# Kernel optimization log

Hardware: AMD Instinct MI355X
Metric: run time of the kernel (lower is better)

The kernel has to match this reference:

```python
import jax, jax.numpy as jnp
import numpy as np

B, C, H, T, K = 32, 128, 512, 8192, 512


def setup_inputs() -> dict:
    key = jax.random.key(0)
    ks = jax.random.split(key, 4)
    s = 0.02
    return {
        "x": jax.random.normal(ks[0], (B, C, T), dtype=jnp.float32),
        "up_w": jax.random.normal(ks[1], (H, C), dtype=jnp.float32) * s,
        "up_b": jnp.zeros((H,), jnp.float32),
        "sal_w": jax.random.normal(ks[2], (H, C), dtype=jnp.float32) * s,
        "sal_b": jnp.zeros((H,), jnp.float32),
        "down_w": jax.random.normal(ks[3], (C, H), dtype=jnp.float32) * s,
        "down_b": jnp.zeros((C,), jnp.float32),
        "k_sparse": K,
    }


def reference(x, up_w, up_b, sal_w, sal_b, down_w, down_b, k_sparse):
    b = x.shape[0]
    # 1x1 Conv1d == per-timestep GEMM
    sig = jnp.einsum('bct,hc->bht', x, up_w) + up_b[None, :, None]   # [B,H,T]
    sal = jnp.einsum('bct,hc->bht', x, sal_w) + sal_b[None, :, None]  # [B,H,T]
    # global softmax over flattened (H*T) per batch item
    flat = jax.nn.softmax(sal.reshape(b, -1), axis=-1)                # [B,H*T]
    # k-sparse: keep top-k values, zero everything else
    vals, idx = jax.lax.top_k(flat, k_sparse)                          # [B,K]
    sparse = jnp.zeros_like(flat).at[jnp.arange(b)[:, None], idx].set(vals)
    sal_sparse = sparse.reshape(sig.shape)                             # [B,H,T]
    gated = sig * sal_sparse                                           # [B,H,T]
    out = jnp.einsum('bht,ch->bct', gated, down_w) + down_b[None, :, None]
    return out
```

## Files before the change

### kernel.cpp

```cpp
#include <hip/hip_runtime.h>
#include <hip/hip_bf16.h>
#include <math.h>

#define BB 32
#define CC 128
#define HH 512
#define TT 8192
#define KMAX 512

#define NBIN 2048
#define CANDCAP 4096
#define HOTCAP 32768
#define TILES 2048
#define TLCAP 256
#define HFLOOR 0.6f
#define BW (0.875f / 2048.0f)
#define INVBW (2048.0f / 0.875f)
#define DELTA_C2 6e-3f
#define DELTA_C1 1.2e-2f

#define N_HIST 0
#define N_SUMEXP 262144
#define N_CANDCNT 262400
#define N_TILECNT 262528
#define N_ZERO 270720
#define N_TAU 270848
#define N_SELCNT 270976
#define N_CELLMAX 271360
#define N_TLIST 8659968
#define N_CANDVAL 10757120
#define N_CANDIDX 11805696
#define N_SELIDX 12329984
#define N_SELVAL 12395520
#define N_SWB 12461056
#define N_XF 12592128
#define N_DWT 79700992
#define N_NEED 79963136

#define O_HIST 0
#define O_SUMEXP 262144
#define O_CANDCNT 262400
#define O_HOTCNT 262528
#define O_ZERO 262656
#define O_TAU 262656
#define O_SELCNT 262784
#define O_CELLMAX 263168
#define O_HOTLIST 8651776
#define O_CANDVAL 8782848
#define O_CANDIDX 9831424
#define O_SELIDX 10355712
#define O_SELVAL 10421248

typedef __attribute__((ext_vector_type(8))) short short8;
typedef __attribute__((ext_vector_type(16))) float f32x16;
typedef __attribute__((address_space(3))) unsigned int lds_u32;
typedef const __attribute__((address_space(1))) unsigned int glb_u32;


__global__ void prep_w(const float* __restrict__ sw, short* __restrict__ swb) {
  int i = blockIdx.x * 256 + threadIdx.x;
  int m = i & 31, u = (i >> 5) & 1, kc = (i >> 6) & 7, w = (i >> 9) & 3, by = i >> 11;
  int h = by * 128 + w * 32 + m;
  int c0 = kc * 16 + u * 8;
  float4 f0 = *(const float4*)(sw + (size_t)h * CC + c0);
  float4 f1 = *(const float4*)(sw + (size_t)h * CC + c0 + 4);
  union { __hip_bfloat162 h2; unsigned u; } p0, p1, p2, p3;
  p0.h2 = __float22bfloat162_rn(make_float2(f0.x, f0.y));
  p1.h2 = __float22bfloat162_rn(make_float2(f0.z, f0.w));
  p2.h2 = __float22bfloat162_rn(make_float2(f1.x, f1.y));
  p3.h2 = __float22bfloat162_rn(make_float2(f1.z, f1.w));
  *(uint4*)(swb + (size_t)i * 8) = make_uint4(p0.u, p1.u, p2.u, p3.u);
}

__global__ void prep_dwt(const float* __restrict__ dw, float* __restrict__ dwt) {
  int i = blockIdx.x * 256 + threadIdx.x;
  int c = i & 127, h = i >> 7;
  dwt[(size_t)h * CC + c] = dw[(size_t)c * HH + h];
}

__global__ __launch_bounds__(256) void prep_xt(const float* __restrict__ x,
                                               short* __restrict__ xf) {
  __shared__ float Lt[128 * 128];
  int tid = threadIdx.x;
  int b = blockIdx.y, bx = blockIdx.x, t0g = bx * 128;
  const float* xb = x + (size_t)b * CC * TT;
  {
    int cq = tid >> 5, tq = tid & 31, t0 = tq * 4;
#pragma unroll
    for (int p = 0; p < 4; p++) {
      int c0 = p * 32 + cq * 4;
      float r0[4], r1[4], r2[4], r3[4];
      *(float4*)r0 = *(const float4*)(xb + (size_t)(c0 + 0) * TT + t0g + t0);
      *(float4*)r1 = *(const float4*)(xb + (size_t)(c0 + 1) * TT + t0g + t0);
      *(float4*)r2 = *(const float4*)(xb + (size_t)(c0 + 2) * TT + t0g + t0);
      *(float4*)r3 = *(const float4*)(xb + (size_t)(c0 + 3) * TT + t0g + t0);
#pragma unroll
      for (int j = 0; j < 4; j++) {
        int t = t0 + j;
        int addr = t * 128 + ((((c0 >> 2) ^ (t & 31)) << 2));
        *(float4*)&Lt[addr] = make_float4(r0[j], r1[j], r2[j], r3[j]);
      }
    }
  }
  __syncthreads();
  int u = tid & 1, m = (tid >> 1) & 31, nt = (tid >> 6) & 3;
  int t = nt * 32 + m;
  short* dst = xf + ((size_t)b * 64 + bx) * 16384 + nt * 4096 + u * 256 + m * 8;
#pragma unroll
  for (int kc = 0; kc < 8; kc++) {
    int c0 = kc * 16 + u * 8;
    float4 f0 = *(float4*)&Lt[t * 128 + ((((c0 >> 2) ^ (t & 31)) << 2))];
    float4 f1 = *(float4*)&Lt[t * 128 + (((((c0 + 4) >> 2) ^ (t & 31)) << 2))];
    union { __hip_bfloat162 h2; unsigned u; } p0, p1, p2, p3;
    p0.h2 = __float22bfloat162_rn(make_float2(f0.x, f0.y));
    p1.h2 = __float22bfloat162_rn(make_float2(f0.z, f0.w));
    p2.h2 = __float22bfloat162_rn(make_float2(f1.x, f1.y));
    p3.h2 = __float22bfloat162_rn(make_float2(f1.z, f1.w));
    *(uint4*)(dst + kc * 512) = make_uint4(p0.u, p1.u, p2.u, p3.u);
  }
}

__global__ __launch_bounds__(256) void pass_a_lds(const short* __restrict__ xf,
                                                  const short* __restrict__ swb,
                                                  const float* __restrict__ sb,
                                                  float* __restrict__ cellmax,
                                                  int* __restrict__ hist,
                                                  double* __restrict__ sumexp) {
  __shared__ short Xs[16384];
  __shared__ double sered[4];
  int tid = threadIdx.x;
  int w = tid >> 6, lane = tid & 63, m = lane & 31, u = lane >> 5;
  int id = blockIdx.x, b = blockIdx.y;
  int bx = ((id >> 5) << 3) | (id & 7);
  int by = (id >> 3) & 3;

  const short* xsl = xf + ((size_t)b * 64 + bx) * 16384;
  {
    const short* gs = xsl + w * 4096 + lane * 8;
    short* ls = &Xs[w * 4096];
#pragma unroll
    for (int i = 0; i < 8; i++) {
      __builtin_amdgcn_global_load_lds((glb_u32*)(gs + i * 512),
                                       (lds_u32*)(ls + i * 512), 16, 0, 0);
    }
  }

  const short* wb_ = swb + (size_t)(by * 4 + w) * 4096 + u * 256 + m * 8;
  short8 afr[8];
#pragma unroll
  for (int kc = 0; kc < 8; kc++) afr[kc] = *(const short8*)(wb_ + kc * 512);

  __syncthreads();

  f32x16 acc0, acc1, acc2, acc3;
#pragma unroll
  for (int r = 0; r < 16; r++) { acc0[r] = 0.f; acc1[r] = 0.f; acc2[r] = 0.f; acc3[r] = 0.f; }

  const short* xr = &Xs[u * 256 + m * 8];
#pragma unroll
  for (int kc = 0; kc < 8; kc++) {
    short8 b0 = *(const short8*)(xr + kc * 512);
    short8 b1 = *(const short8*)(xr + 4096 + kc * 512);
    short8 b2 = *(const short8*)(xr + 8192 + kc * 512);
    short8 b3 = *(const short8*)(xr + 12288 + kc * 512);
    acc0 = __builtin_amdgcn_mfma_f32_32x32x16_bf16(afr[kc], b0, acc0, 0, 0, 0);
    acc1 = __builtin_amdgcn_mfma_f32_32x32x16_bf16(afr[kc], b1, acc1, 0, 0, 0);
    acc2 = __builtin_amdgcn_mfma_f32_32x32x16_bf16(afr[kc], b2, acc2, 0, 0, 0);
    acc3 = __builtin_amdgcn_mfma_f32_32x32x16_bf16(afr[kc], b3, acc3, 0, 0, 0);
  }

  int h0 = by * 128;
  float tmax = -1e30f;
  float se = 0.f;
#define EPI(ACC)                                                              \
  {                                                                           \
    _Pragma("unroll") for (int g = 0; g < 4; g++) {                           \
      float bias4[4];                                                         \
      *(float4*)bias4 = *(const float4*)&sb[h0 + w * 32 + g * 8 + u * 4];     \
      _Pragma("unroll") for (int q = 0; q < 4; q++) {                         \
        float s = ACC[g * 4 + q] + bias4[q];                                  \
        tmax = fmaxf(tmax, s);                                                \
        se += __expf(s);                                                      \
        if (s >= HFLOOR) {                                                    \
          int bin = (int)((s - HFLOOR) * INVBW);                              \
          if (bin > NBIN - 1) bin = NBIN - 1;                                 \
          atomicAdd(&hist[b * NBIN + bin], 1);                                \
        }                                                                     \
      }                                                                       \
    }                                                                         \
  }
  EPI(acc0) EPI(acc1) EPI(acc2) EPI(acc3)
#undef EPI
  int cid = ((b * 4 + by) * 64 + bx) * 256 + tid;
  cellmax[cid] = tmax;
  double sed = (double)se;
#pragma unroll
  for (int mm = 1; mm < 64; mm <<= 1) sed += __shfl_xor(sed, mm);
  if (lane == 0) sered[w] = sed;
  __syncthreads();
  if (tid == 0) atomicAdd(&sumexp[b], sered[0] + sered[1] + sered[2] + sered[3]);
}

__global__ void pass_b(const int* __restrict__ hist, float* __restrict__ tau,
                       const int* __restrict__ kptr) {
  __shared__ int hsh[NBIN];
  __shared__ int ps[256];
  int b = blockIdx.x, tid = threadIdx.x;
  int part = 0;
#pragma unroll
  for (int j = 0; j < 8; j++) {
    int v = hist[b * NBIN + tid * 8 + j];
    hsh[tid * 8 + j] = v;
    part += v;
  }
  ps[tid] = part;
  __syncthreads();
  if (tid == 0) {
    int k = kptr[0];
    if (k < 1) k = 1;
    if (k > KMAX) k = KMAX;
    long cum = 0;
    float tv = HFLOOR;
    for (int i = 255; i >= 0; i--) {
      if (cum + ps[i] >= k) {
        long r = k - cum;
        long c2 = 0;
        for (int j = 7; j >= 0; j--) {
          c2 += hsh[i * 8 + j];
          if (c2 >= r) { tv = HFLOOR + (i * 8 + j) * BW; break; }
        }
        break;
      }
      cum += ps[i];
    }
    tau[b] = tv;
  }
}

__global__ void pass_c1_fast(const float* __restrict__ cellmax, const float* __restrict__ tau,
                             int* __restrict__ tilecnt, int* __restrict__ tlist) {
  int i = blockIdx.x * blockDim.x + threadIdx.x;
  float v = cellmax[i];
  int b = i >> 16;
  if (v >= tau[b] - DELTA_C1) {
    int tile = (b << 6) | ((i >> 8) & 63);
    int pos = atomicAdd(&tilecnt[tile], 1);
    if (pos < TLCAP) tlist[tile * TLCAP + pos] = i;
  }
}

__global__ __launch_bounds__(512, 2) void pass_c2_fast(
    const float* __restrict__ x, const float* __restrict__ sw,
    const float* __restrict__ sb, const float* __restrict__ tau,
    const int* __restrict__ tilecnt, const int* __restrict__ tlist,
    int* __restrict__ candcnt, double* __restrict__ candval, int* __restrict__ candidx) {
  __shared__ float Xt[128 * 132];
  int tile = blockIdx.x;
  int b = tile >> 6, bx = tile & 63;
  int cnt = tilecnt[tile];
  if (cnt <= 0) return;
  if (cnt > TLCAP) cnt = TLCAP;
  int tid = threadIdx.x;
  {
    int cq = tid >> 5, tq = tid & 31, t4 = tq * 4;
    int sw4 = ((t4 >> 5) & 3) << 2;
    const float* xb = x + (size_t)b * CC * TT + bx * 128;
#pragma unroll
    for (int p = 0; p < 8; p++) {
      int c = p * 16 + cq;
      float4 v = *(const float4*)(xb + (size_t)c * TT + t4);
      int cc = c ^ sw4;
      Xt[(t4 + 0) * 132 + cc] = v.x;
      Xt[(t4 + 1) * 132 + cc] = v.y;
      Xt[(t4 + 2) * 132 + cc] = v.z;
      Xt[(t4 + 3) * 132 + cc] = v.w;
    }
  }
  __syncthreads();
  int wv = tid >> 6, lane = tid & 63;
  int nt = lane >> 4, r = lane & 15;
  int swz = nt << 2;
  float tmb = tau[b] - DELTA_C2;
  int tbase = tile * TLCAP;
  if (wv >= cnt) return;

#define DEC(CID)                                                        \
  {                                                                     \
    int by_ = ((CID) >> 14) & 3, ta_ = (CID) & 255;                     \
    int w_ = ta_ >> 6, lc_ = ta_ & 63, m_ = lc_ & 31, u_ = lc_ >> 5;    \
    h = by_ * 128 + w_ * 32 + (r >> 2) * 8 + (r & 3) + 4 * u_;          \
    t = bx * 128 + nt * 32 + m_;                                        \
    swp = (const float4*)(sw + (size_t)h * CC);                         \
    xrp = &Xt[(nt * 32 + m_) * 132];                                    \
    sbh = sb[h];                                                        \
  }
#define ISSUE(WB, XB, CH)                                               \
  _Pragma("unroll") for (int j = 0; j < 8; j++) {                       \
    WB[j] = swp[(CH) * 8 + j];                                          \
    XB[j] = *(const float4*)(xrp + (((CH) * 32 + j * 4) ^ swz));        \
  }
#define DOT(WB, XB)                                                     \
  _Pragma("unroll") for (int j = 0; j < 8; j++) {                       \
    a0 = fma((double)XB[j].x, (double)WB[j].x, a0);                     \
    a1 = fma((double)XB[j].y, (double)WB[j].y, a1);                     \
    a2 = fma((double)XB[j].z, (double)WB[j].z, a2);                     \
    a3 = fma((double)XB[j].w, (double)WB[j].w, a3);                     \
  }

  float4 wA[8], xA[8], wB[8], xB[8];
  int h, t;
  const float4* swp;
  const float* xrp;
  float sbh;
  int s = wv;
  int cid = tlist[tbase + s];
  DEC(cid);
  ISSUE(wA, xA, 0);
  for (; s < cnt; ) {
    int sn = s + 8;
    int cidN = (sn < cnt) ? tlist[tbase + sn] : cid;
    double a0 = 0.0, a1 = 0.0, a2 = 0.0, a3 = 0.0;
    ISSUE(wB, xB, 1); DOT(wA, xA);
    ISSUE(wA, xA, 2); DOT(wB, xB);
    ISSUE(wB, xB, 3); DOT(wA, xA);
    int hO = h, tO = t;
    float sbO = sbh;
    if (sn < cnt) { cid = cidN; DEC(cid); }
    ISSUE(wA, xA, 0); DOT(wB, xB);
    double acc = a0 + a1 + a2 + a3 + (double)sbO;
    if (acc >= (double)tmb) {
      int pos = atomicAdd(&candcnt[b], 1);
      if (pos < CANDCAP) {
        candval[b * CANDCAP + pos] = acc;
        candidx[b * CANDCAP + pos] = hO * TT + tO;
      }
    }
    s = sn;
  }
#undef DEC
#undef ISSUE
#undef DOT
}

__global__ void pass_d(const int* __restrict__ candcnt, const double* __restrict__ candval,
                       const int* __restrict__ candidx, const double* __restrict__ sumexp,
                       const int* __restrict__ kptr, int* __restrict__ selidx,
                       float* __restrict__ selval, int* __restrict__ selcnt) {
  __shared__ double sv[CANDCAP];
  __shared__ int si[CANDCAP];
  int b = blockIdx.x;
  int n = candcnt[b];
  if (n > CANDCAP) n = CANDCAP;
  int k = kptr[0];
  if (k < 0) k = 0;
  if (k > KMAX) k = KMAX;
  for (int i = threadIdx.x; i < n; i += blockDim.x) {
    sv[i] = candval[b * CANDCAP + i];
    si[i] = candidx[b * CANDCAP + i];
  }
  __syncthreads();
  double S = sumexp[b];
  for (int i = threadIdx.x; i < n; i += blockDim.x) {
    double vi = sv[i];
    int ii = si[i];
    int rank = 0;
    for (int q = 0; q < n; q++) {
      double vq = sv[q];
      rank += (vq > vi) || (vq == vi && si[q] < ii);
    }
    if (rank < k) {
      selidx[b * KMAX + rank] = ii;
      selval[b * KMAX + rank] = (float)(exp(vi) / S);
    }
  }
  if (threadIdx.x == 0) selcnt[b] = n < k ? n : k;
}

__global__ void pass_e1(const float* __restrict__ db, float* __restrict__ out) {
  int row = blockIdx.x;
  int c = row & (CC - 1);
  float v = db[c];
  float4 v4 = make_float4(v, v, v, v);
  float4* o = (float4*)(out + (size_t)row * TT);
#pragma unroll
  for (int q = 0; q < 8; q++) o[q * 256 + threadIdx.x] = v4;
}

__global__ void pass_e2_fast(const short* __restrict__ xf, const float* __restrict__ uw,
                             const float* __restrict__ ub, const float* __restrict__ dwt,
                             const int* __restrict__ selidx, const float* __restrict__ selval,
                             const int* __restrict__ selcnt, float* __restrict__ out) {
  int b = blockIdx.y, j = blockIdx.x;
  if (j >= selcnt[b]) return;
  int idx = selidx[b * KMAX + j];
  float val = selval[b * KMAX + j];
  int h = idx >> 13, t = idx & (TT - 1);
  int bx = t >> 7, tl = t & 127, nt = tl >> 5, m = tl & 31;
  int lane = threadIdx.x;
  const short* xt = xf + ((size_t)b * 64 + bx) * 16384 + nt * 4096 + m * 8;
  int off = (lane >> 3) * 512 + ((lane >> 2) & 1) * 256 + (lane & 3) * 2;
  __hip_bfloat162 hv = *(const __hip_bfloat162*)(xt + off);
  float2 xv = __bfloat1622float2(hv);
  int c0 = lane * 2;
  float2 wv = *(const float2*)(uw + (size_t)h * CC + c0);
  float p = xv.x * wv.x + xv.y * wv.y;
#pragma unroll
  for (int mm = 1; mm < 64; mm <<= 1) p += __shfl_xor(p, mm);
  float sig = p + ub[h];
  float g = sig * val;
  float2 dv = *(const float2*)(dwt + (size_t)h * CC + c0);
  atomicAdd(&out[((size_t)b * CC + c0) * TT + t], g * dv.x);
  atomicAdd(&out[((size_t)b * CC + c0 + 1) * TT + t], g * dv.y);
}

__global__ __launch_bounds__(256) void pass_a_slow(const float* __restrict__ x,
                                                   const float* __restrict__ sw,
                                                   const float* __restrict__ sb,
                                                   float* __restrict__ cellmax,
                                                   int* __restrict__ hist,
                                                   double* __restrict__ sumexp) {
  __shared__ short Ws[128 * 128];
  __shared__ short Xs[128 * 128];
  __shared__ float sbs[128];
  int tid = threadIdx.x;
  int b = blockIdx.z, by = blockIdx.y, bx = blockIdx.x;
  int h0 = by * 128, t0g = bx * 128;
  const float* xb = x + (size_t)b * CC * TT;
  {
    int cq = tid >> 5, tq = tid & 31;
    int t0 = tq * 4;
#pragma unroll
    for (int p = 0; p < 4; p++) {
      int c0 = p * 32 + cq * 4;
      float r0[4], r1[4], r2[4], r3[4];
      *(float4*)r0 = *(const float4*)(xb + (size_t)(c0 + 0) * TT + t0g + t0);
      *(float4*)r1 = *(const float4*)(xb + (size_t)(c0 + 1) * TT + t0g + t0);
      *(float4*)r2 = *(const float4*)(xb + (size_t)(c0 + 2) * TT + t0g + t0);
      *(float4*)r3 = *(const float4*)(xb + (size_t)(c0 + 3) * TT + t0g + t0);
#pragma unroll
      for (int j = 0; j < 4; j++) {
        int t = t0 + j;
        int addr = t * 128 + ((((c0 >> 3) ^ (t & 15)) << 3) | (c0 & 7));
        union { __hip_bfloat162 h; unsigned int u; } a0, a1;
        a0.h = __float22bfloat162_rn(make_float2(r0[j], r1[j]));
        a1.h = __float22bfloat162_rn(make_float2(r2[j], r3[j]));
        *(uint2*)&Xs[addr] = make_uint2(a0.u, a1.u);
      }
    }
  }
  {
    int hh = tid >> 1, c4 = (tid & 1) << 2;
#pragma unroll
    for (int k = 0; k < 16; k++) {
      int c0 = k * 8 + c4;
      float r[4];
      *(float4*)r = *(const float4*)(sw + (size_t)(h0 + hh) * CC + c0);
      int addr = hh * 128 + ((((c0 >> 3) ^ (hh & 15)) << 3) | (c0 & 7));
      union { __hip_bfloat162 h; unsigned int u; } a0, a1;
      a0.h = __float22bfloat162_rn(make_float2(r[0], r[1]));
      a1.h = __float22bfloat162_rn(make_float2(r[2], r[3]));
      *(uint2*)&Ws[addr] = make_uint2(a0.u, a1.u);
    }
  }
  if (tid < 128) sbs[tid] = sb[h0 + tid];
  __syncthreads();
  int w = tid >> 6, lane = tid & 63, m = lane & 31, u = lane >> 5;
  f32x16 acc0, acc1, acc2, acc3;
#pragma unroll
  for (int r = 0; r < 16; r++) { acc0[r] = 0.f; acc1[r] = 0.f; acc2[r] = 0.f; acc3[r] = 0.f; }
  const short* wrow = &Ws[(w * 32 + m) * 128];
  const short* xrow = &Xs[m * 128];
#pragma unroll
  for (int kc = 0; kc < 8; kc++) {
    int pc = ((((kc << 1) | u) ^ (m & 15)) << 3);
    short8 af = *(const short8*)(wrow + pc);
    short8 b0 = *(const short8*)(xrow + 0 * 32 * 128 + pc);
    short8 b1 = *(const short8*)(xrow + 1 * 32 * 128 + pc);
    short8 b2 = *(const short8*)(xrow + 2 * 32 * 128 + pc);
    short8 b3 = *(const short8*)(xrow + 3 * 32 * 128 + pc);
    acc0 = __builtin_amdgcn_mfma_f32_32x32x16_bf16(af, b0, acc0, 0, 0, 0);
    acc1 = __builtin_amdgcn_mfma_f32_32x32x16_bf16(af, b1, acc1, 0, 0, 0);
    acc2 = __builtin_amdgcn_mfma_f32_32x32x16_bf16(af, b2, acc2, 0, 0, 0);
    acc3 = __builtin_amdgcn_mfma_f32_32x32x16_bf16(af, b3, acc3, 0, 0, 0);
  }
  float tmax = -1e30f;
  float se = 0.f;
#define EPI(ACC)                                                              \
  {                                                                           \
    _Pragma("unroll") for (int g = 0; g < 4; g++) {                           \
      float bias4[4];                                                         \
      *(float4*)bias4 = *(float4*)&sbs[w * 32 + g * 8 + u * 4];               \
      _Pragma("unroll") for (int q = 0; q < 4; q++) {                         \
        float s = ACC[g * 4 + q] + bias4[q];                                  \
        tmax = fmaxf(tmax, s);                                                \
        se += __expf(s);                                                      \
        if (s >= HFLOOR) {                                                    \
          int bin = (int)((s - HFLOOR) * INVBW);                              \
          if (bin > NBIN - 1) bin = NBIN - 1;                                 \
          atomicAdd(&hist[b * NBIN + bin], 1);                                \
        }                                                                     \
      }                                                                       \
    }                                                                         \
  }
  EPI(acc0) EPI(acc1) EPI(acc2) EPI(acc3)
#undef EPI
  int cid = ((b * 4 + by) * 64 + bx) * 256 + tid;
  cellmax[cid] = tmax;
  double sed = (double)se;
#pragma unroll
  for (int mm = 1; mm < 64; mm <<= 1) sed += __shfl_xor(sed, mm);
  if ((tid & 63) == 0) atomicAdd(&sumexp[b], sed);
}

__global__ void pass_c1_slow(const float* __restrict__ cellmax, const float* __restrict__ tau,
                             int* __restrict__ hotcnt, int* __restrict__ hotlist) {
  int i = blockIdx.x * blockDim.x + threadIdx.x;
  float v = cellmax[i];
  int b = i >> 16;
  if (v >= tau[b] - DELTA_C1) {
    int pos = atomicAdd(hotcnt, 1);
    if (pos < HOTCAP) hotlist[pos] = i;
  }
}

__global__ void pass_c2_slow(const float* __restrict__ x, const float* __restrict__ sw,
                             const float* __restrict__ sb, const float* __restrict__ tau,
                             const int* __restrict__ hotcnt, const int* __restrict__ hotlist,
                             int* __restrict__ candcnt, double* __restrict__ candval,
                             int* __restrict__ candidx) {
  int j = blockIdx.x;
  int n = hotcnt[0];
  if (n > HOTCAP) n = HOTCAP;
  if (j >= n) return;
  int cid = hotlist[j];
  int b = cid >> 16, by = (cid >> 14) & 3, bx = (cid >> 8) & 63;
  int ta = cid & 255;
  int w = ta >> 6, lane = ta & 63, m = lane & 31, u = lane >> 5;
  int e = threadIdx.x;
  int nt = e >> 4, r = e & 15;
  int h = by * 128 + w * 32 + (r >> 2) * 8 + (r & 3) + 4 * u;
  int t = bx * 128 + nt * 32 + m;
  const float* xb = x + (size_t)b * CC * TT;
  double acc = 0.0;
#pragma unroll 8
  for (int c = 0; c < CC; c++)
    acc += (double)xb[(size_t)c * TT + t] * (double)sw[h * CC + c];
  acc += (double)sb[h];
  float tm = tau[b] - DELTA_C2;
  if (acc >= (double)tm) {
    int pos = atomicAdd(&candcnt[b], 1);
    if (pos < CANDCAP) {
      candval[b * CANDCAP + pos] = acc;
      candidx[b * CANDCAP + pos] = h * TT + t;
    }
  }
}

__global__ void pass_e2_slow(const float* __restrict__ x, const float* __restrict__ uw,
                             const float* __restrict__ ub, const float* __restrict__ dw,
                             const int* __restrict__ selidx, const float* __restrict__ selval,
                             const int* __restrict__ selcnt, float* __restrict__ out) {
  int b = blockIdx.y, j = blockIdx.x;
  if (j >= selcnt[b]) return;
  int idx = selidx[b * KMAX + j];
  float val = selval[b * KMAX + j];
  int h = idx >> 13, t = idx & (TT - 1);
  int c = threadIdx.x;
  const float* xb = x + (size_t)b * CC * TT;
  float p = xb[(size_t)c * TT + t] * uw[h * CC + c] +
            xb[(size_t)(c + 64) * TT + t] * uw[h * CC + c + 64];
#pragma unroll
  for (int m = 1; m < 64; m <<= 1) p += __shfl_xor(p, m);
  float sig = p + ub[h];
  float g = sig * val;
  atomicAdd(&out[((size_t)b * CC + c) * TT + t], g * dw[c * HH + h]);
  atomicAdd(&out[((size_t)b * CC + c + 64) * TT + t], g * dw[(c + 64) * HH + h]);
}

extern "C" void kernel_launch(void* const* d_in, const int* in_sizes, int n_in,
                              void* d_out, int out_size, void* d_ws, size_t ws_size,
                              hipStream_t stream) {
  const float* x = (const float*)d_in[0];
  const float* uw = (const float*)d_in[1];
  const float* ub = (const float*)d_in[2];
  const float* sw = (const float*)d_in[3];
  const float* sb = (const float*)d_in[4];
  const float* dw = (const float*)d_in[5];
  const float* db = (const float*)d_in[6];
  const int* kptr = (const int*)d_in[7];
  float* out = (float*)d_out;
  char* ws = (char*)d_ws;

  if (ws_size >= (size_t)N_NEED) {
    int* hist = (int*)(ws + N_HIST);
    double* sumexp = (double*)(ws + N_SUMEXP);
    int* candcnt = (int*)(ws + N_CANDCNT);
    int* tilecnt = (int*)(ws + N_TILECNT);
    float* tau = (float*)(ws + N_TAU);
    int* selcnt = (int*)(ws + N_SELCNT);
    float* cellmax = (float*)(ws + N_CELLMAX);
    int* tlist = (int*)(ws + N_TLIST);
    double* candval = (double*)(ws + N_CANDVAL);
    int* candidx = (int*)(ws + N_CANDIDX);
    int* selidx = (int*)(ws + N_SELIDX);
    float* selval = (float*)(ws + N_SELVAL);
    short* swb = (short*)(ws + N_SWB);
    short* xf = (short*)(ws + N_XF);
    float* dwt = (float*)(ws + N_DWT);

    (void)hipMemsetAsync(d_ws, 0, N_ZERO, stream);
    prep_w<<<32, 256, 0, stream>>>(sw, swb);
    prep_dwt<<<256, 256, 0, stream>>>(dw, dwt);
    prep_xt<<<dim3(64, 32), 256, 0, stream>>>(x, xf);
    pass_a_lds<<<dim3(256, 32), 256, 0, stream>>>(xf, swb, sb, cellmax, hist, sumexp);
    pass_b<<<32, 256, 0, stream>>>(hist, tau, kptr);
    pass_c1_fast<<<8192, 256, 0, stream>>>(cellmax, tau, tilecnt, tlist);
    pass_c2_fast<<<TILES, 512, 0, stream>>>(x, sw, sb, tau, tilecnt, tlist, candcnt,
                                            candval, candidx);
    pass_d<<<32, 256, 0, stream>>>(candcnt, candval, candidx, sumexp, kptr, selidx,
                                   selval, selcnt);
    pass_e1<<<BB * CC, 256, 0, stream>>>(db, out);
    pass_e2_fast<<<dim3(KMAX, BB), 64, 0, stream>>>(xf, uw, ub, dwt, selidx, selval,
                                                    selcnt, out);
  } else {
    int* hist = (int*)(ws + O_HIST);
    double* sumexp = (double*)(ws + O_SUMEXP);
    int* candcnt = (int*)(ws + O_CANDCNT);
    int* hotcnt = (int*)(ws + O_HOTCNT);
    float* tau = (float*)(ws + O_TAU);
    int* selcnt = (int*)(ws + O_SELCNT);
    float* cellmax = (float*)(ws + O_CELLMAX);
    int* hotlist = (int*)(ws + O_HOTLIST);
    double* candval = (double*)(ws + O_CANDVAL);
    int* candidx = (int*)(ws + O_CANDIDX);
    int* selidx = (int*)(ws + O_SELIDX);
    float* selval = (float*)(ws + O_SELVAL);

    (void)hipMemsetAsync(d_ws, 0, O_ZERO, stream);
    pass_a_slow<<<dim3(64, 4, 32), 256, 0, stream>>>(x, sw, sb, cellmax, hist, sumexp);
    pass_b<<<32, 256, 0, stream>>>(hist, tau, kptr);
    pass_c1_slow<<<8192, 256, 0, stream>>>(cellmax, tau, hotcnt, hotlist);
    pass_c2_slow<<<HOTCAP, 64, 0, stream>>>(x, sw, sb, tau, hotcnt, hotlist, candcnt,
                                            candval, candidx);
    pass_d<<<32, 256, 0, stream>>>(candcnt, candval, candidx, sumexp, kptr, selidx,
                                   selval, selcnt);
    pass_e1<<<BB * CC, 256, 0, stream>>>(db, out);
    pass_e2_slow<<<dim3(KMAX, BB), 64, 0, stream>>>(x, uw, ub, dw, selidx, selval,
                                                    selcnt, out);
  }
}
```

Before: 942.9 us.

## Stage salience weight rows through LDS with coalesced loads in candidate recompute

Each wave now loads its 16 weight rows with coalesced float4 global loads into a per-wave LDS buffer (padded stride 33), then reads them from LDS in the double-precision dot product. Previously each lane streamed its own weight row straight from global memory in strided chunks. The next candidate's weights are prefetched into registers while the current one is computed. Launch bounds drop to one block per SM because the extra LDS (about 67 KB) plus Xt no longer fits two blocks. This trades occupancy for better-coalesced global traffic.

```diff
diff --git a/kernel.cpp b/kernel.cpp
--- a/kernel.cpp
+++ b/kernel.cpp
@@ -249,12 +249,13 @@
   }
 }
 
-__global__ __launch_bounds__(512, 2) void pass_c2_fast(
+__global__ __launch_bounds__(512, 1) void pass_c2_fast(
     const float* __restrict__ x, const float* __restrict__ sw,
     const float* __restrict__ sb, const float* __restrict__ tau,
     const int* __restrict__ tilecnt, const int* __restrict__ tlist,
     int* __restrict__ candcnt, double* __restrict__ candval, int* __restrict__ candidx) {
   __shared__ float Xt[128 * 132];
+  __shared__ float4 Wsh[8 * 16 * 33];
   int tile = blockIdx.x;
   int b = tile >> 6, bx = tile & 63;
   int cnt = tilecnt[tile];
@@ -278,68 +279,89 @@
   }
   __syncthreads();
   int wv = tid >> 6, lane = tid & 63;
+  if (wv >= cnt) return;
   int nt = lane >> 4, r = lane & 15;
   int swz = nt << 2;
   float tmb = tau[b] - DELTA_C2;
   int tbase = tile * TLCAP;
-  if (wv >= cnt) return;
-
-#define DEC(CID)                                                        \
-  {                                                                     \
-    int by_ = ((CID) >> 14) & 3, ta_ = (CID) & 255;                     \
-    int w_ = ta_ >> 6, lc_ = ta_ & 63, m_ = lc_ & 31, u_ = lc_ >> 5;    \
-    h = by_ * 128 + w_ * 32 + (r >> 2) * 8 + (r & 3) + 4 * u_;          \
-    t = bx * 128 + nt * 32 + m_;                                        \
-    swp = (const float4*)(sw + (size_t)h * CC);                         \
-    xrp = &Xt[(nt * 32 + m_) * 132];                                    \
-    sbh = sb[h];                                                        \
-  }
-#define ISSUE(WB, XB, CH)                                               \
-  _Pragma("unroll") for (int j = 0; j < 8; j++) {                       \
-    WB[j] = swp[(CH) * 8 + j];                                          \
-    XB[j] = *(const float4*)(xrp + (((CH) * 32 + j * 4) ^ swz));        \
-  }
-#define DOT(WB, XB)                                                     \
-  _Pragma("unroll") for (int j = 0; j < 8; j++) {                       \
-    a0 = fma((double)XB[j].x, (double)WB[j].x, a0);                     \
-    a1 = fma((double)XB[j].y, (double)WB[j].y, a1);                     \
-    a2 = fma((double)XB[j].z, (double)WB[j].z, a2);                     \
-    a3 = fma((double)XB[j].w, (double)WB[j].w, a3);                     \
-  }
-
-  float4 wA[8], xA[8], wB[8], xB[8];
-  int h, t;
-  const float4* swp;
+  float4* Ws = &Wsh[wv * 528];
+  int hi = lane >> 5, col4 = lane & 31;
+
+#define DEC(CID)                                                         \
+  {                                                                      \
+    int by_ = ((CID) >> 14) & 3, ta_ = (CID) & 255;                      \
+    int w_ = ta_ >> 6, lc_ = ta_ & 63, m_ = lc_ & 31, u_ = lc_ >> 5;     \
+    hbase = by_ * 128 + w_ * 32 + 4 * u_;                                \
+    h = hbase + (r >> 2) * 8 + (r & 3);                                  \
+    t = bx * 128 + nt * 32 + m_;                                         \
+    xrp = &Xt[(nt * 32 + m_) * 132];                                     \
+    sbh = sb[h];                                                         \
+  }
+#define LOADW(G)                                                         \
+  _Pragma("unroll") for (int i = 0; i < 8; i++) {                        \
+    int row_ = i * 2 + hi;                                               \
+    int h_ = hbase + ((row_ >> 2) << 3) + (row_ & 3);                    \
+    G[i] = *(const float4*)(sw + (size_t)h_ * CC + col4 * 4);            \
+  }
+#define WRITEW(G)                                                        \
+  _Pragma("unroll") for (int i = 0; i < 8; i++) {                        \
+    Ws[(i * 2 + hi) * 33 + col4] = G[i];                                 \
+  }
+#define DOTEMIT(XRP, HC, TC, SBC)                                        \
+  {                                                                      \
+    double a0 = 0.0, a1 = 0.0, a2 = 0.0, a3 = 0.0;                       \
+    _Pragma("unroll") for (int j = 0; j < 32; j++) {                     \
+      float4 w4 = Ws[r * 33 + j];                                        \
+      float4 x4 = *(const float4*)((XRP) + ((j * 4) ^ swz));             \
+      a0 = fma((double)x4.x, (double)w4.x, a0);                          \
+      a1 = fma((double)x4.y, (double)w4.y, a1);                          \
+      a2 = fma((double)x4.z, (double)w4.z, a2);                          \
+      a3 = fma((double)x4.w, (double)w4.w, a3);                          \
+    }                                                                    \
+    double acc = a0 + a1 + a2 + a3 + (double)(SBC);                      \
+    if (acc >= (double)tmb) {                                            \
+      int pos = atomicAdd(&candcnt[b], 1);                               \
+      if (pos < CANDCAP) {                                               \
+        candval[b * CANDCAP + pos] = acc;                                \
+        candidx[b * CANDCAP + pos] = (HC) * TT + (TC);                   \
+      }                                                                  \
+    }                                                                    \
+  }
+
+  float4 gA[8], gB[8];
+  int h, t, hbase;
   const float* xrp;
   float sbh;
   int s = wv;
   int cid = tlist[tbase + s];
   DEC(cid);
-  ISSUE(wA, xA, 0);
-  for (; s < cnt; ) {
-    int sn = s + 8;
-    int cidN = (sn < cnt) ? tlist[tbase + sn] : cid;
-    double a0 = 0.0, a1 = 0.0, a2 = 0.0, a3 = 0.0;
-    ISSUE(wB, xB, 1); DOT(wA, xA);
-    ISSUE(wA, xA, 2); DOT(wB, xB);
-    ISSUE(wB, xB, 3); DOT(wA, xA);
-    int hO = h, tO = t;
-    float sbO = sbh;
-    if (sn < cnt) { cid = cidN; DEC(cid); }
-    ISSUE(wA, xA, 0); DOT(wB, xB);
-    double acc = a0 + a1 + a2 + a3 + (double)sbO;
-    if (acc >= (double)tmb) {
-      int pos = atomicAdd(&candcnt[b], 1);
-      if (pos < CANDCAP) {
-        candval[b * CANDCAP + pos] = acc;
-        candidx[b * CANDCAP + pos] = hO * TT + tO;
-      }
-    }
-    s = sn;
+  LOADW(gA);
+  while (true) {
+    WRITEW(gA);
+    {
+      const float* xrpC = xrp; int hC = h, tC = t; float sbC = sbh;
+      int sn = s + 8;
+      bool more = sn < cnt;
+      if (more) { cid = tlist[tbase + sn]; DEC(cid); LOADW(gB); }
+      DOTEMIT(xrpC, hC, tC, sbC);
+      s = sn;
+      if (!more) break;
+    }
+    WRITEW(gB);
+    {
+      const float* xrpC = xrp; int hC = h, tC = t; float sbC = sbh;
+      int sn = s + 8;
+      bool more = sn < cnt;
+      if (more) { cid = tlist[tbase + sn]; DEC(cid); LOADW(gA); }
+      DOTEMIT(xrpC, hC, tC, sbC);
+      s = sn;
+      if (!more) break;
+    }
   }
 #undef DEC
-#undef ISSUE
-#undef DOT
+#undef LOADW
+#undef WRITEW
+#undef DOTEMIT
 }
 
 __global__ void pass_d(const int* __restrict__ candcnt, const double* __restrict__ candval,
```

Measured after the change: 924.7 us. Within noise of the previous version (-1.9%).
